# Optimization experiments

Hardware: AMD Instinct MI355X
Metric: run time of the kernel (lower is better)

The kernel has to match this reference:

```python
import jax, jax.numpy as jnp
import numpy as np

N = 30000      # nodes
IN = 768       # input feature dim
C = 128        # hidden channels (= conv out_dim, = gate dim)
HEADS = 4      # attention heads (TransformerConv and Semantic)
DH = 128       # per-head dim (concat=False -> out_channels)
R = 3          # num relations
E = 80000      # edges per relation
NEG = 0.01     # LeakyReLU slope


def setup_inputs() -> dict:
    key = jax.random.key(0)
    ks = iter(jax.random.split(key, 64))
    def nx(shape):
        return jax.random.normal(next(ks), shape, dtype=jnp.float32) * 0.02
    inp = {}
    inp["x"] = jax.random.normal(next(ks), (N, IN), dtype=jnp.float32)
    inp["edges"] = jax.random.randint(next(ks), (R, 2, E), 0, N, dtype=jnp.int32)
    inp["lin1_W"] = nx((IN, C)); inp["lin1_b"] = jnp.zeros((C,), jnp.float32)
    for l in ("l1", "l2"):
        inp[f"{l}_Wq"] = nx((R, C, HEADS * DH)); inp[f"{l}_bq"] = jnp.zeros((R, HEADS * DH), jnp.float32)
        inp[f"{l}_Wk"] = nx((R, C, HEADS * DH)); inp[f"{l}_bk"] = jnp.zeros((R, HEADS * DH), jnp.float32)
        inp[f"{l}_Wv"] = nx((R, C, HEADS * DH)); inp[f"{l}_bv"] = jnp.zeros((R, HEADS * DH), jnp.float32)
        inp[f"{l}_Ws"] = nx((R, C, DH));         inp[f"{l}_bs"] = jnp.zeros((R, DH), jnp.float32)
        inp[f"{l}_gW"] = nx((C + DH, C));        inp[f"{l}_gb"] = jnp.zeros((C,), jnp.float32)
        inp[f"{l}_sW1"] = nx((HEADS, C, C));     inp[f"{l}_sb1"] = jnp.zeros((HEADS, C), jnp.float32)
        inp[f"{l}_sw2"] = nx((HEADS, C))
    inp["lin2_W"] = nx((C, C)); inp["lin2_b"] = jnp.zeros((C,), jnp.float32)
    inp["clf_W"] = nx((C, 2)); inp["clf_b"] = jnp.zeros((2,), jnp.float32)
    return inp


def lrelu(x):
    return jnp.where(x >= 0, x, NEG * x)


def transformer_conv(x, src, dst, Wq, bq, Wk, bk, Wv, bv, Ws, bs):
    # PyG TransformerConv, heads=HEADS, concat=False (head mean), root_weight=True, eval (no dropout)
    n = x.shape[0]
    q = (x @ Wq + bq).reshape(n, HEADS, DH)
    k = (x @ Wk + bk).reshape(n, HEADS, DH)
    v = (x @ Wv + bv).reshape(n, HEADS, DH)
    logits = (q[dst] * k[src]).sum(-1) / np.sqrt(DH)      # [E, H]
    m = jax.ops.segment_max(logits, dst, num_segments=n)  # scatter-softmax (stable)
    a = jnp.exp(logits - m[dst])
    s = jax.ops.segment_sum(a, dst, num_segments=n)
    alpha = a / s[dst]
    agg = jax.ops.segment_sum(alpha[:, :, None] * v[src], dst, num_segments=n)  # [N, H, DH]
    return agg.mean(axis=1) + x @ Ws + bs


def semantic(Hm, sW1, sb1, sw2):
    # Hm: [N, R, C]; per-head scoring MLP -> softmax over relations -> weighted sum, averaged over heads
    t = jnp.tanh(jnp.einsum('nrc,hco->hnro', Hm, sW1) + sb1[:, None, None, :])  # [H, N, R, C]
    scores = jnp.einsum('hnro,ho->hnr', t, sw2).mean(axis=1)                    # [H, R]
    beta = jax.nn.softmax(scores, axis=-1)
    return jnp.einsum('hr,nrc->nc', beta, Hm) / HEADS


def rgt_layer(x, edges, Wq, bq, Wk, bk, Wv, bv, Ws, bs, gW, gb, sW1, sb1, sw2):
    Hs = []
    for r in range(R):  # small fixed relation loop
        src, dst = edges[r, 0], edges[r, 1]
        U = transformer_conv(x, src, dst, Wq[r], bq[r], Wk[r], bk[r], Wv[r], bv[r], Ws[r], bs[r])
        Z = jax.nn.sigmoid(jnp.concatenate([U, x], axis=1) @ gW + gb)
        Hs.append(jnp.tanh(U) * Z + x * (1.0 - Z))
    Hm = jnp.stack(Hs, axis=1)  # [N, R, C]
    return semantic(Hm, sW1, sb1, sw2)


def reference(x, edges, lin1_W, lin1_b,
              l1_Wq, l1_bq, l1_Wk, l1_bk, l1_Wv, l1_bv, l1_Ws, l1_bs, l1_gW, l1_gb, l1_sW1, l1_sb1, l1_sw2,
              l2_Wq, l2_bq, l2_Wk, l2_bk, l2_Wv, l2_bv, l2_Ws, l2_bs, l2_gW, l2_gb, l2_sW1, l2_sb1, l2_sw2,
              lin2_W, lin2_b, clf_W, clf_b):
    h = lrelu(x @ lin1_W + lin1_b)
    h = rgt_layer(h, edges, l1_Wq, l1_bq, l1_Wk, l1_bk, l1_Wv, l1_bv, l1_Ws, l1_bs, l1_gW, l1_gb, l1_sW1, l1_sb1, l1_sw2)
    h = rgt_layer(h, edges, l2_Wq, l2_bq, l2_Wk, l2_bk, l2_Wv, l2_bv, l2_Ws, l2_bs, l2_gW, l2_gb, l2_sW1, l2_sb1, l2_sw2)
    h = lrelu(h @ lin2_W + lin2_b)
    return h @ clf_W + clf_b
```

## Files before the change

kernel.cpp:

```cpp
#include <hip/hip_runtime.h>
#include <math.h>

#define Nn 30000
#define RR 3
#define EE 80000
#define MT_M 235

#define SAP 72
#define EP_LD 68
#define KBIG 0x40000000

typedef __attribute__((ext_vector_type(8))) short bf16x8;
typedef __attribute__((ext_vector_type(4))) float f32x4;

__device__ __forceinline__ unsigned short f2bf(float f) {
    union { float f; unsigned u; } v; v.f = f;
    unsigned r = v.u + 0x7fff + ((v.u >> 16) & 1);
    return (unsigned short)(r >> 16);
}
__device__ __forceinline__ float bf2f(short h) {
    union { unsigned u; float f; } v;
    v.u = ((unsigned)(unsigned short)h) << 16;
    return v.f;
}
__device__ __forceinline__ float fast_tanh(float x) {
    float e = __expf(2.f * x);
    return 1.f - 2.f / (e + 1.f);
}
__device__ __forceinline__ void unpack8(uint4 u, float* f) {
    union { unsigned u; float f; } a;
    a.u = u.x << 16;          f[0] = a.f;
    a.u = u.x & 0xffff0000u;  f[1] = a.f;
    a.u = u.y << 16;          f[2] = a.f;
    a.u = u.y & 0xffff0000u;  f[3] = a.f;
    a.u = u.z << 16;          f[4] = a.f;
    a.u = u.z & 0xffff0000u;  f[5] = a.f;
    a.u = u.w << 16;          f[6] = a.f;
    a.u = u.w & 0xffff0000u;  f[7] = a.f;
}

__device__ __forceinline__ void mfma_core(
    const short* __restrict__ A, int lda,
    const short* __restrict__ A2, int lda2, int ksplit,
    const short* __restrict__ Bt,
    int M, int K, int m0, int n0,
    short* As, short* Bs, f32x4 (&acc)[4][4])
{
    const int t = threadIdx.x;
    const int srow = t >> 3;
    const int scol = (t & 7) << 3;
    const int lane = t & 63;
    const int wave = t >> 6;
    const int wm = (wave >> 1) << 6;
    const int wn = (wave & 1) << 6;
    const int fr = lane & 15;
    const int quad = lane >> 4;

    for (int k0 = 0; k0 < K; k0 += 64) {
        const short* Abase; int kk0, ldax;
        if (k0 < ksplit) { Abase = A;  kk0 = k0;          ldax = lda;  }
        else             { Abase = A2; kk0 = k0 - ksplit; ldax = lda2; }
        #pragma unroll
        for (int rr = 0; rr < 4; rr++) {
            int r = srow + rr * 32;
            int gr = m0 + r;
            bf16x8 va = {0, 0, 0, 0, 0, 0, 0, 0};
            if (gr < M) va = *(const bf16x8*)(Abase + (size_t)gr * ldax + kk0 + scol);
            *(bf16x8*)(As + r * SAP + scol) = va;
        }
        #pragma unroll
        for (int rr = 0; rr < 4; rr++) {
            int r = srow + rr * 32;
            bf16x8 vb = *(const bf16x8*)(Bt + (size_t)(n0 + r) * K + k0 + scol);
            *(bf16x8*)(Bs + r * SAP + scol) = vb;
        }
        __syncthreads();
// ... 27 lines not shown
    __shared__ short As[128 * SAP];
    __shared__ short Bs[128 * SAP];
    f32x4 acc[4][4];
    #pragma unroll
    for (int i = 0; i < 4; i++)
        #pragma unroll
        for (int j = 0; j < 4; j++) acc[i][j] = (f32x4){0.f, 0.f, 0.f, 0.f};
    int m0 = blockIdx.y * 128, n0 = blockIdx.x * 128;
    mfma_core(A, lda, A2, lda2, ksplit, Bt, M, K, m0, n0, As, Bs, acc);

    const int t = threadIdx.x;
    const int lane = t & 63, wave = t >> 6;
    const int wm = (wave >> 1) << 6, wn = (wave & 1) << 6;
    const int fr = lane & 15, quad = lane >> 4;
    float* ws = (float*)As + wave * 16 * EP_LD;
    const int rrow = lane >> 2;
    const int cseg = (lane & 3) << 4;
    #pragma unroll
    for (int mi = 0; mi < 4; mi++) {
        #pragma unroll
        for (int ni = 0; ni < 4; ni++)
            #pragma unroll
            for (int reg = 0; reg < 4; reg++)
                ws[(quad * 4 + reg) * EP_LD + ni * 16 + fr] = acc[mi][ni][reg];
        int gr = m0 + wm + mi * 16 + rrow;
        if (gr >= M) continue;
        int gc = n0 + wn + cseg;
        float vals[16];
        #pragma unroll
        for (int j = 0; j < 16; j++) {
            float v = ws[rrow * EP_LD + cseg + j] + bias[gc + j];
            if (act == 1) v = (v >= 0.f) ? v : 0.01f * v;
            vals[j] = v;
        }
        if (C) {
            float* cp = C + (size_t)gr * ldc + gc;
            #pragma unroll
            for (int j4 = 0; j4 < 4; j4++)
                *(float4*)(cp + j4 * 4) = make_float4(vals[j4 * 4], vals[j4 * 4 + 1],
                                                      vals[j4 * 4 + 2], vals[j4 * 4 + 3]);
        }
        if (Cbf) {
            unsigned pk[8];
            #pragma unroll
            for (int j2 = 0; j2 < 8; j2++)
                pk[j2] = ((unsigned)f2bf(vals[2 * j2 + 1]) << 16) | (unsigned)f2bf(vals[2 * j2]);
            unsigned* bp = (unsigned*)(Cbf + (size_t)gr * ldcbf + gc);
            *(uint4*)bp       = make_uint4(pk[0], pk[1], pk[2], pk[3]);
            *(uint4*)(bp + 4) = make_uint4(pk[4], pk[5], pk[6], pk[7]);
        }
    }
}

__global__ __launch_bounds__(256) void gemm_qkvs(
    const short* __restrict__ A,
    const short* __restrict__ Wt, const float* __restrict__ bias,
    short* __restrict__ qkv3, short* __restrict__ Ubf, int M)
{
    __shared__ short As[128 * SAP];
    __shared__ short Bs[128 * SAP];
    f32x4 acc[4][4];
    #pragma unroll
    for (int i = 0; i < 4; i++)
        #pragma unroll
        for (int j = 0; j < 4; j++) acc[i][j] = (f32x4){0.f, 0.f, 0.f, 0.f};
    int m0 = blockIdx.y * 128, bx = blockIdx.x, n0 = bx * 128;
    mfma_core(A, 128, A, 128, KBIG, Wt, M, 128, m0, n0, As, Bs, acc);

    const int t = threadIdx.x;
    const int lane = t & 63, wave = t >> 6;
    const int wm = (wave >> 1) << 6, wn = (wave & 1) << 6;
    const int fr = lane & 15, quad = lane >> 4;
    float* ws = (float*)As + wave * 16 * EP_LD;
    const int rrow = lane >> 2;
    const int cseg = (lane & 3) << 4;
    #pragma unroll
    for (int mi = 0; mi < 4; mi++) {
        #pragma unroll
        for (int ni = 0; ni < 4; ni++)
            #pragma unroll
            for (int reg = 0; reg < 4; reg++)
                ws[(quad * 4 + reg) * EP_LD + ni * 16 + fr] = acc[mi][ni][reg];
        int gr = m0 + wm + mi * 16 + rrow;
        if (gr >= M) continue;
        int lc = wn + cseg;
        float vals[16];
        #pragma unroll
        for (int j = 0; j < 16; j++)
            vals[j] = ws[rrow * EP_LD + cseg + j] + bias[n0 + lc + j];
        unsigned pk[8];
        #pragma unroll
        for (int j2 = 0; j2 < 8; j2++)
            pk[j2] = ((unsigned)f2bf(vals[2 * j2 + 1]) << 16) | (unsigned)f2bf(vals[2 * j2]);
        short* dst;
        if (bx < 36) {
            int r = bx / 12;
            dst = qkv3 + ((size_t)(r * Nn + gr)) * 1536 + (bx - r * 12) * 128 + lc;
        } else {
            dst = Ubf + (size_t)gr * 384 + (bx - 36) * 128 + lc;
        }
        unsigned* bp = (unsigned*)dst;
        *(uint4*)bp       = make_uint4(pk[0], pk[1], pk[2], pk[3]);
        *(uint4*)(bp + 4) = make_uint4(pk[4], pk[5], pk[6], pk[7]);
    }
}

__global__ __launch_bounds__(256) void gate_mfma(
    const short* __restrict__ Ubf,
    const short* __restrict__ Hbf,
    const short* __restrict__ gWt, const float* __restrict__ gb,
    const float* __restrict__ Hf,
    float* __restrict__ Hm, short* __restrict__ HmBf,
    int M)
{
    __shared__ short As[128 * SAP];
    __shared__ short Bs[128 * SAP];
    f32x4 acc[4][4];
    #pragma unroll
    for (int i = 0; i < 4; i++)
        #pragma unroll
        for (int j = 0; j < 4; j++) acc[i][j] = (f32x4){0.f, 0.f, 0.f, 0.f};
    int r = blockIdx.z;
    int m0 = blockIdx.y * 128;
    mfma_core(Ubf + r * 128, 384, Hbf, 128, 128, gWt, M, 256, m0, 0, As, Bs, acc);

    const int t = threadIdx.x;
    const int lane = t & 63, wave = t >> 6;
    const int wm = (wave >> 1) << 6, wn = (wave & 1) << 6;
    const int fr = lane & 15, quad = lane >> 4;
    float* ws = (float*)As + wave * 16 * EP_LD;
    const int rrow = lane >> 2;
    const int cseg = (lane & 3) << 4;
    #pragma unroll
    for (int mi = 0; mi < 4; mi++) {
        #pragma unroll
        for (int ni = 0; ni < 4; ni++)
            #pragma unroll
            for (int reg = 0; reg < 4; reg++)
                ws[(quad * 4 + reg) * EP_LD + ni * 16 + fr] = acc[mi][ni][reg];
        int gr = m0 + wm + mi * 16 + rrow;
        if (gr >= M) continue;
        int gc = wn + cseg;
        const short* up = Ubf + (size_t)gr * 384 + r * 128 + gc;
        const float* hp = Hf + (size_t)gr * 128 + gc;
        float uv[16], hv[16];
        uint4 u0 = *(const uint4*)up;
        uint4 u1 = *(const uint4*)(up + 8);
        unpack8(u0, uv); unpack8(u1, uv + 8);
        #pragma unroll
        for (int j4 = 0; j4 < 4; j4++)
            *(float4*)(hv + j4 * 4) = *(const float4*)(hp + j4 * 4);
        float vals[16];
        #pragma unroll
        for (int j = 0; j < 16; j++) {
            float g = ws[rrow * EP_LD + cseg + j] + gb[gc + j];
            float z = 1.f / (1.f + __expf(-g));
// ... 80 lines not shown
            float e0 = __expf(s0 - mx), e1 = __expf(s1 - mx), e2 = __expf(s2 - mx);
            float inv = 1.f / (e0 + e1 + e2);
            wr[0] += 0.25f * e0 * inv;
            wr[1] += 0.25f * e1 * inv;
            wr[2] += 0.25f * e2 * inv;
        }
        w[0] = wr[0]; w[1] = wr[1]; w[2] = wr[2];
    }
}

__global__ void mix_kernel(const float* __restrict__ Hm, const float* __restrict__ w,
                           float* __restrict__ h, short* __restrict__ hbf, int total4)
{
    int i = blockIdx.x * blockDim.x + threadIdx.x;
    if (i >= total4) return;
    int n = i >> 5, c4 = (i & 31) << 2;
    const float* row = Hm + (size_t)n * 384 + c4;
    float4 a = *(const float4*)row;
    float4 b = *(const float4*)(row + 128);
    float4 c = *(const float4*)(row + 256);
    float w0 = w[0], w1 = w[1], w2 = w[2];
    float4 v = make_float4(w0 * a.x + w1 * b.x + w2 * c.x,
                           w0 * a.y + w1 * b.y + w2 * c.y,
                           w0 * a.z + w1 * b.z + w2 * c.z,
                           w0 * a.w + w1 * b.w + w2 * c.w);
    *(float4*)(h + (size_t)n * 128 + c4) = v;
    unsigned p0 = ((unsigned)f2bf(v.y) << 16) | (unsigned)f2bf(v.x);
    unsigned p1 = ((unsigned)f2bf(v.w) << 16) | (unsigned)f2bf(v.z);
    *(uint2*)(hbf + (size_t)n * 128 + c4) = make_uint2(p0, p1);
}

__global__ void convert_bf16_kernel(const float* __restrict__ src, unsigned* __restrict__ dst, int n_pairs)
{
    int i = blockIdx.x * blockDim.x + threadIdx.x;
    if (i >= n_pairs) return;
    float2 f = ((const float2*)src)[i];
    dst[i] = ((unsigned)f2bf(f.y) << 16) | (unsigned)f2bf(f.x);
}

__global__ void prep_global_kernel(const float* __restrict__ lin1_W, const float* __restrict__ lin2_W,
                                   short* __restrict__ lin1Wt, short* __restrict__ lin2Wt)
{
    int id = blockIdx.x * blockDim.x + threadIdx.x;
    if (id < 98304) {
        int n = id / 768, k = id % 768;
        lin1Wt[id] = (short)f2bf(lin1_W[k * 128 + n]);
    } else if (id < 114688) {
        int r = id - 98304;
        int n = r / 128, k = r % 128;
        lin2Wt[r] = (short)f2bf(lin2_W[k * 128 + n]);
    }
}

__global__ void prep_layer_kernel(
    const float* __restrict__ Wq, const float* __restrict__ Wk, const float* __restrict__ Wv,
    const float* __restrict__ Ws, const float* __restrict__ bq, const float* __restrict__ bk,
    const float* __restrict__ bv, const float* __restrict__ bs,
    const float* __restrict__ gW, const float* __restrict__ sW1,
    short* __restrict__ qkvsWt, short* __restrict__ gWt,
    short* __restrict__ sW1t, float* __restrict__ qkvsB)
{
    const int S0 = 638976;
    const int S1 = S0 + 32768;
    const int S2 = S1 + 65536;
    const int S3 = S2 + 4992;
    int id = blockIdx.x * blockDim.x + threadIdx.x;
    if (id < S0) {
        int n = id / 128, k = id - n * 128;
        float v;
        if (n < 4608) {
            int r = n / 1536, j = n - r * 1536;
            if (j < 512)       v = Wq[(size_t)r * 65536 + k * 512 + j];
            else if (j < 1024) v = Wk[(size_t)r * 65536 + k * 512 + (j - 512)];
            else               v = Wv[(size_t)r * 65536 + k * 512 + (j - 1024)];
        } else {
            int m = n - 4608;
            int r = m / 128, c = m - r * 128;
            v = Ws[(size_t)r * 16384 + k * 128 + c];
        }
        qkvsWt[id] = (short)f2bf(v);
    } else if (id < S1) {
        int q = id - S0;
        int n = q / 256, k = q - n * 256;
        gWt[q] = (short)f2bf(gW[k * 128 + n]);
    } else if (id < S2) {
        int q = id - S1;
        int h = q / 16384, rem = q - h * 16384;
        int n = rem / 128, k = rem - n * 128;
        sW1t[q] = (short)f2bf(sW1[(size_t)h * 16384 + k * 128 + n]);
    } else if (id < S3) {
        int q = id - S2;
        float v;
        if (q < 4608) {
            int r = q / 1536, j = q - r * 1536;
            if (j < 512)       v = bq[r * 512 + j];
            else if (j < 1024) v = bk[r * 512 + (j - 512)];
            else               v = bv[r * 512 + (j - 1024)];
        } else {
            v = bs[q - 4608];
        }
        qkvsB[q] = v;
    }
}

__global__ void zero_i32_kernel(int* __restrict__ p, int n)
{
    int i = blockIdx.x * blockDim.x + threadIdx.x;
    if (i < n) p[i] = 0;
}

__global__ void hist3_kernel(const int* __restrict__ edges, int* __restrict__ cnt3)
{
    int i = blockIdx.x * blockDim.x + threadIdx.x;
    if (i >= 3 * EE) return;
    int r = i / EE, e = i - r * EE;
    int d = edges[(size_t)r * 2 * EE + EE + e];
    atomicAdd(&cnt3[r * Nn + d], 1);
}

__global__ __launch_bounds__(1024) void scan3_kernel(const int* __restrict__ cnt3,
                                                     int* __restrict__ rowptr3)
{
    __shared__ int part[1024];
    const int r = blockIdx.x;
    const int* cnt = cnt3 + r * Nn;
    int* rowptr = rowptr3 + r * (Nn + 1);
    int tid = threadIdx.x;
    int per = (Nn + 1023) >> 10;
    int base = tid * per;
    int s = 0;
    for (int i = 0; i < per; i++) {
        int idx = base + i;
        if (idx < Nn) s += cnt[idx];
    }
    part[tid] = s;
    __syncthreads();
    for (int off = 1; off < 1024; off <<= 1) {
        int val = (tid >= off) ? part[tid - off] : 0;
        __syncthreads();
        part[tid] += val;
        __syncthreads();
    }
    int excl = (tid == 0) ? 0 : part[tid - 1];
    for (int i = 0; i < per; i++) {
        int idx = base + i;
        if (idx < Nn) { rowptr[idx] = excl; excl += cnt[idx]; }
    }
    if (tid == 1023) rowptr[Nn] = part[1023];
}

__global__ void scatter3_kernel(const int* __restrict__ edges,
                                const int* __restrict__ rowptr3, int* __restrict__ fill3,
                                int* __restrict__ col3)
{
    int i = blockIdx.x * blockDim.x + threadIdx.x;
    if (i >= 3 * EE) return;
    int r = i / EE, e = i - r * EE;
    int src = edges[(size_t)r * 2 * EE + e];
    int d   = edges[(size_t)r * 2 * EE + EE + e];
    int pos = rowptr3[r * (Nn + 1) + d] + atomicAdd(&fill3[r * Nn + d], 1);
    col3[r * EE + pos] = src;
}

__global__ __launch_bounds__(256) void attn_kernel(
    const short* __restrict__ qkv3,
    const int* __restrict__ rowptr3, const int* __restrict__ col3,
    short* __restrict__ Ubf)
{
    int wid = ((blockIdx.x * blockDim.x + threadIdx.x) >> 6);
    int lane = threadIdx.x & 63;
    if (wid >= 3 * Nn) return;
    int r = wid / Nn, n = wid - r * Nn;
    const short* qkv = qkv3 + (size_t)r * Nn * 1536;
    const int* rowptr = rowptr3 + r * (Nn + 1);
    const int* colb = col3 + r * EE;
    int beg = rowptr[n], end = rowptr[n + 1];

    uint4 qv = ((const uint4*)(qkv + (size_t)n * 1536))[lane];
    float qf[8];
    unpack8(qv, qf);

    float m = -INFINITY, s = 0.f;
    float acc[8] = {0.f, 0.f, 0.f, 0.f, 0.f, 0.f, 0.f, 0.f};
    const float scale = 0.088388347648318447f;

    for (int i = beg; i < end; i++) {
        int src = colb[i];
        const short* base = qkv + (size_t)src * 1536;
        uint4 kv4 = ((const uint4*)(base + 512))[lane];
        uint4 vv4 = ((const uint4*)(base + 1024))[lane];
        float kf[8];
        unpack8(kv4, kf);
        float p = qf[0] * kf[0] + qf[1] * kf[1] + qf[2] * kf[2] + qf[3] * kf[3]
                + qf[4] * kf[4] + qf[5] * kf[5] + qf[6] * kf[6] + qf[7] * kf[7];
        p += __shfl_xor(p, 1);
        p += __shfl_xor(p, 2);
        p += __shfl_xor(p, 4);
        p += __shfl_xor(p, 8);
        float l = p * scale;
        float nm = fmaxf(m, l);
        float sc = __expf(m - nm);
        float pe = __expf(l - nm);
        float vf[8];
        unpack8(vv4, vf);
        s = s * sc + pe;
        #pragma unroll
        for (int j = 0; j < 8; j++) acc[j] = acc[j] * sc + pe * vf[j];
        m = nm;
    }

    float inv = (s > 0.f) ? 1.f / s : 0.f;
    #pragma unroll
    for (int j = 0; j < 8; j++) acc[j] *= inv;
    #pragma unroll
    for (int j = 0; j < 8; j++) acc[j] += __shfl_xor(acc[j], 16);
    #pragma unroll
    for (int j = 0; j < 8; j++) acc[j] += __shfl_xor(acc[j], 32);

    if (lane < 16) {
        short* urow = Ubf + (size_t)n * 384 + r * 128 + lane * 8;
        uint4 old = *(uint4*)urow;
        float sv[8];
        unpack8(old, sv);
        #pragma unroll
        for (int j = 0; j < 8; j++) sv[j] += 0.25f * acc[j];
        unsigned p0 = ((unsigned)f2bf(sv[1]) << 16) | (unsigned)f2bf(sv[0]);
        unsigned p1 = ((unsigned)f2bf(sv[3]) << 16) | (unsigned)f2bf(sv[2]);
        unsigned p2 = ((unsigned)f2bf(sv[5]) << 16) | (unsigned)f2bf(sv[4]);
        unsigned p3 = ((unsigned)f2bf(sv[7]) << 16) | (unsigned)f2bf(sv[6]);
        *(uint4*)urow = make_uint4(p0, p1, p2, p3);
    }
}

__global__ void clf_kernel(const float* __restrict__ t, const float* __restrict__ W,
                           const float* __restrict__ b, float* __restrict__ out, int M)
{
    int n = blockIdx.x * blockDim.x + threadIdx.x;
    if (n >= M) return;
    const float* row = t + (size_t)n * 128;
    float a0 = b[0], a1 = b[1];
    #pragma unroll
    for (int kk = 0; kk < 128; kk++) {
        float a = row[kk];
        a0 += a * W[kk * 2];
        a1 += a * W[kk * 2 + 1];
    }
    out[n * 2] = a0;
    out[n * 2 + 1] = a1;
}

extern "C" void kernel_launch(void* const* d_in, const int* in_sizes, int n_in,
                              void* d_out, int out_size, void* d_ws, size_t ws_size,
                              hipStream_t stream)
{
    const float* x      = (const float*)d_in[0];
    const int*   edges  = (const int*)d_in[1];
    const float* lin1_W = (const float*)d_in[2];
    const float* lin1_b = (const float*)d_in[3];
    const int L0 = 4, L1 = 17;
    const float* lin2_W = (const float*)d_in[30];
    const float* lin2_b = (const float*)d_in[31];
    const float* clf_W  = (const float*)d_in[32];
    const float* clf_b  = (const float*)d_in[33];
    float* out = (float*)d_out;

    char* w = (char*)d_ws;
    size_t off = 0;
    auto alloc = [&](size_t bytes) { void* p = w + off; off = (off + bytes + 255) & ~(size_t)255; return p; };
    float* h      = (float*)alloc((size_t)Nn * 128 * 4);
    short* h_bf   = (short*)alloc((size_t)Nn * 128 * 2);
    short* U_bf   = (short*)alloc((size_t)Nn * 384 * 2);
    char* BIG     = (char*)alloc((size_t)3 * Nn * 1536 * 2);
    short* qkv3   = (short*)BIG;
    short* x_bf   = (short*)BIG;
    float* Hm     = (float*)BIG;
    short* Hm_bf  = (short*)(BIG + (size_t)Nn * 384 * 4);
    float* lin2o  = (float*)BIG;
    short* lin1Wt = (short*)alloc((size_t)98304 * 2);
    short* lin2Wt = (short*)alloc((size_t)16384 * 2);
    short* qkvsWt = (short*)alloc((size_t)2 * 638976 * 2);
    short* gWt    = (short*)alloc((size_t)2 * 32768 * 2);
    short* sW1t   = (short*)alloc((size_t)2 * 65536 * 2);
    float* qkvsB  = (float*)alloc((size_t)2 * 4992 * 4);
    int* rowptr3  = (int*)alloc((size_t)3 * (Nn + 1) * 4);
    int* cnt3     = (int*)alloc((size_t)3 * Nn * 4);
    int* col3     = (int*)alloc((size_t)3 * EE * 4);
    float* partial = (float*)alloc((size_t)12 * MT_M * 4);
    float* scores = (float*)alloc(12 * 4);
    float* wmix   = (float*)alloc(3 * 4);

    const int MT = MT_M;
    dim3 blk(256);

    {
        int n_pairs = Nn * 768 / 2;
        convert_bf16_kernel<<<(n_pairs + 255) / 256, blk, 0, stream>>>(x, (unsigned*)x_bf, n_pairs);
        prep_global_kernel<<<(114688 + 255) / 256, blk, 0, stream>>>(lin1_W, lin2_W, lin1Wt, lin2Wt);
        for (int l = 0; l < 2; l++) {
            int base = (l == 0) ? L0 : L1;
            prep_layer_kernel<<<(742272 + 255) / 256, blk, 0, stream>>>(
                (const float*)d_in[base + 0], (const float*)d_in[base + 2], (const float*)d_in[base + 4],
                (const float*)d_in[base + 6], (const float*)d_in[base + 1], (const float*)d_in[base + 3],
                (const float*)d_in[base + 5], (const float*)d_in[base + 7],
                (const float*)d_in[base + 8], (const float*)d_in[base + 10],
                qkvsWt + (size_t)l * 638976, gWt + (size_t)l * 32768,
                sW1t + (size_t)l * 65536, qkvsB + (size_t)l * 4992);
        }
        zero_i32_kernel<<<(3 * Nn + 255) / 256, blk, 0, stream>>>(cnt3, 3 * Nn);
        hist3_kernel<<<(3 * EE + 255) / 256, blk, 0, stream>>>(edges, cnt3);
        scan3_kernel<<<3, 1024, 0, stream>>>(cnt3, rowptr3);
        zero_i32_kernel<<<(3 * Nn + 255) / 256, blk, 0, stream>>>(cnt3, 3 * Nn);
        scatter3_kernel<<<(3 * EE + 255) / 256, blk, 0, stream>>>(edges, rowptr3, cnt3, col3);
    }

    gemm_mfma<<<dim3(1, MT), blk, 0, stream>>>(
        x_bf, 768, x_bf, 768, KBIG, lin1Wt, lin1_b, h, 128, h_bf, 128, Nn, 768, 1);

    for (int l = 0; l < 2; l++) {
        int base = (l == 0) ? L0 : L1;
        const float* gb  = (const float*)d_in[base + 9];
        const float* sb1 = (const float*)d_in[base + 11];
        const float* sw2 = (const float*)d_in[base + 12];
        short* lqkvsWt = qkvsWt + (size_t)l * 638976;
        short* lgWt    = gWt + (size_t)l * 32768;
        short* lsW1t   = sW1t + (size_t)l * 65536;
        float* lqkvsB  = qkvsB + (size_t)l * 4992;

        gemm_qkvs<<<dim3(39, MT), blk, 0, stream>>>(
            h_bf, lqkvsWt, lqkvsB, qkv3, U_bf, Nn);

        attn_kernel<<<(3 * Nn + 3) / 4, blk, 0, stream>>>(qkv3, rowptr3, col3, U_bf);

        gate_mfma<<<dim3(1, MT, 3), blk, 0, stream>>>(
            U_bf, h_bf, lgWt, gb, h, Hm, Hm_bf, Nn);

        semantic_mfma<<<dim3(4, MT, 3), blk, 0, stream>>>(Hm_bf, lsW1t, sb1, sw2, partial, Nn);
        reduce12_kernel<<<12, 64, 0, stream>>>(partial, scores);
        compute_w_kernel<<<1, 64, 0, stream>>>(scores, wmix, 1.f / (float)Nn);
        mix_kernel<<<(Nn * 32 + 255) / 256, blk, 0, stream>>>(Hm, wmix, h, h_bf, Nn * 32);
    }

    gemm_mfma<<<dim3(1, MT), blk, 0, stream>>>(
        h_bf, 128, h_bf, 128, KBIG, lin2Wt, lin2_b, lin2o, 128, (short*)nullptr, 0, Nn, 128, 1);
    clf_kernel<<<(Nn + 255) / 256, blk, 0, stream>>>(lin2o, clf_W, clf_b, out, Nn);
}
```

Baseline: 975.4 us.

## Keep QKVS weight tile in registers and loop over five row tiles per block

Replaces the LDS-staged QKVS projection GEMM with a register-resident version. Each block loads its 128x128 weight slice into registers once and reuses it across five 128-row tiles of the input. A fragments are read straight from global memory, which removes shared-memory staging and barriers. The epilogue writes bf16 directly from MFMA accumulators using swapped operands and the hardware packed convert. The cost is much higher register pressure (launch bounds of 256,2), fewer blocks, and direct global A loads that are less coalesced.

```diff
diff --git a/kernel.cpp b/kernel.cpp
--- a/kernel.cpp
+++ b/kernel.cpp
@@ -155,56 +155,95 @@
     }
 }
 
-__global__ __launch_bounds__(256) void gemm_qkvs(
+__global__ __launch_bounds__(256, 2) void gemm_qkvs_v2(
     const short* __restrict__ A,
-    const short* __restrict__ Wt, const float* __restrict__ bias,
+    const short* __restrict__ Bt,
+    const float* __restrict__ bias,
     short* __restrict__ qkv3, short* __restrict__ Ubf, int M)
 {
-    __shared__ short As[128 * SAP];
-    __shared__ short Bs[128 * SAP];
-    f32x4 acc[4][4];
-    #pragma unroll
-    for (int i = 0; i < 4; i++)
-        #pragma unroll
-        for (int j = 0; j < 4; j++) acc[i][j] = (f32x4){0.f, 0.f, 0.f, 0.f};
-    int m0 = blockIdx.y * 128, bx = blockIdx.x, n0 = bx * 128;
-    mfma_core(A, 128, A, 128, KBIG, Wt, M, 128, m0, n0, As, Bs, acc);
-
-    const int t = threadIdx.x;
-    const int lane = t & 63, wave = t >> 6;
-    const int wm = (wave >> 1) << 6, wn = (wave & 1) << 6;
-    const int fr = lane & 15, quad = lane >> 4;
-    float* ws = (float*)As + wave * 16 * EP_LD;
-    const int rrow = lane >> 2;
-    const int cseg = (lane & 3) << 4;
-    #pragma unroll
-    for (int mi = 0; mi < 4; mi++) {
-        #pragma unroll
-        for (int ni = 0; ni < 4; ni++)
-            #pragma unroll
-            for (int reg = 0; reg < 4; reg++)
-                ws[(quad * 4 + reg) * EP_LD + ni * 16 + fr] = acc[mi][ni][reg];
-        int gr = m0 + wm + mi * 16 + rrow;
-        if (gr >= M) continue;
-        int lc = wn + cseg;
-        float vals[16];
-        #pragma unroll
-        for (int j = 0; j < 16; j++)
-            vals[j] = ws[rrow * EP_LD + cseg + j] + bias[n0 + lc + j];
-        unsigned pk[8];
-        #pragma unroll
-        for (int j2 = 0; j2 < 8; j2++)
-            pk[j2] = ((unsigned)f2bf(vals[2 * j2 + 1]) << 16) | (unsigned)f2bf(vals[2 * j2]);
-        short* dst;
-        if (bx < 36) {
-            int r = bx / 12;
-            dst = qkv3 + ((size_t)(r * Nn + gr)) * 1536 + (bx - r * 12) * 128 + lc;
-        } else {
-            dst = Ubf + (size_t)gr * 384 + (bx - 36) * 128 + lc;
-        }
-        unsigned* bp = (unsigned*)dst;
-        *(uint4*)bp       = make_uint4(pk[0], pk[1], pk[2], pk[3]);
-        *(uint4*)(bp + 4) = make_uint4(pk[4], pk[5], pk[6], pk[7]);
+    const int tt = blockIdx.x;
+    const int n0 = tt * 128;
+    const int lane = threadIdx.x & 63;
+    const int wave = threadIdx.x >> 6;
+    const int wm = (wave >> 1) << 6;
+    const int wn = (wave & 1) << 6;
+    const int fr = lane & 15;
+    const int quad = lane >> 4;
+
+    bf16x8 bq[4][4];
+    #pragma unroll
+    for (int ni = 0; ni < 4; ni++)
+        #pragma unroll
+        for (int kc = 0; kc < 4; kc++)
+            bq[ni][kc] = *(const bf16x8*)(Bt + (size_t)(n0 + wn + ni * 16 + fr) * 128
+                                              + kc * 32 + quad * 8);
+
+    float4 b4[4];
+    #pragma unroll
+    for (int ni = 0; ni < 4; ni++)
+        b4[ni] = *(const float4*)(bias + n0 + wn + ni * 16 + quad * 4);
+
+    short* outBase;
+    size_t rowStride, colOff;
+    if (tt < 36) {
+        int r3 = tt / 12;
+        outBase = qkv3 + (size_t)r3 * Nn * 1536;
+        rowStride = 1536;
+        colOff = (size_t)(tt - r3 * 12) * 128;
+    } else {
+        outBase = Ubf;
+        rowStride = 384;
+        colOff = (size_t)(tt - 36) * 128;
+    }
+
+    #pragma unroll 1
+    for (int p = 0; p < 5; p++) {
+        const int m0 = (blockIdx.y * 5 + p) * 128;
+
+        bf16x8 af[4][4];
+        #pragma unroll
+        for (int mi = 0; mi < 4; mi++) {
+            int gr = m0 + wm + mi * 16 + fr;
+            #pragma unroll
+            for (int kc = 0; kc < 4; kc++) {
+                bf16x8 v = {0, 0, 0, 0, 0, 0, 0, 0};
+                if (gr < M) v = *(const bf16x8*)(A + (size_t)gr * 128 + kc * 32 + quad * 8);
+                af[mi][kc] = v;
+            }
+        }
+
+        f32x4 acc[4][4];
+        #pragma unroll
+        for (int i = 0; i < 4; i++)
+            #pragma unroll
+            for (int j = 0; j < 4; j++) acc[i][j] = (f32x4){0.f, 0.f, 0.f, 0.f};
+
+        #pragma unroll
+        for (int kc = 0; kc < 4; kc++)
+            #pragma unroll
+            for (int mi = 0; mi < 4; mi++)
+                #pragma unroll
+                for (int ni = 0; ni < 4; ni++)
+                    acc[mi][ni] = __builtin_amdgcn_mfma_f32_16x16x32_bf16(
+                        bq[ni][kc], af[mi][kc], acc[mi][ni], 0, 0, 0);
+
+        #pragma unroll
+        for (int mi = 0; mi < 4; mi++) {
+            int gr = m0 + wm + mi * 16 + fr;
+            if (gr >= M) continue;
+            short* dst = outBase + (size_t)gr * rowStride + colOff + wn;
+            #pragma unroll
+            for (int ni = 0; ni < 4; ni++) {
+                float v0 = acc[mi][ni][0] + b4[ni].x;
+                float v1 = acc[mi][ni][1] + b4[ni].y;
+                float v2 = acc[mi][ni][2] + b4[ni].z;
+                float v3 = acc[mi][ni][3] + b4[ni].w;
+                unsigned u0, u1;
+                asm("v_cvt_pk_bf16_f32 %0, %1, %2" : "=v"(u0) : "v"(v0), "v"(v1));
+                asm("v_cvt_pk_bf16_f32 %0, %1, %2" : "=v"(u1) : "v"(v2), "v"(v3));
+                *(uint2*)(dst + ni * 16 + quad * 4) = make_uint2(u0, u1);
+            }
+        }
     }
 }
 
@@ -665,7 +704,7 @@
         short* lsW1t   = sW1t + (size_t)l * 65536;
         float* lqkvsB  = qkvsB + (size_t)l * 4992;
 
-        gemm_qkvs<<<dim3(39, MT), blk, 0, stream>>>(
+        gemm_qkvs_v2<<<dim3(39, 47), blk, 0, stream>>>(
             h_bf, lqkvsWt, lqkvsB, qkv3, U_bf, Nn);
 
         attn_kernel<<<(3 * Nn + 3) / 4, blk, 0, stream>>>(qkv3, rowptr3, col3, U_bf);
```

Measured after the change: 1.013 ms. 3.9% more time.

## Reuse staged A tile across three output column tiles in QKV GEMM

Applied to the files above, without the earlier changes.

The QKV/skip projection GEMM now stages the 128x128 activation tile in shared memory once per block and loops over three 128-column weight tiles. It reads the B fragments straight from global memory into registers, so B no longer goes through shared memory. This cuts redundant A loads and launches a third as many blocks. In exchange there is less parallelism (13 blocks across instead of 39), higher register pressure from the held B fragments, and more shared memory per block.

```diff
diff --git a/kernel.cpp b/kernel.cpp
--- a/kernel.cpp
+++ b/kernel.cpp
@@ -8,6 +8,7 @@
 
 #define SAP 72
 #define EP_LD 68
+#define AS3 136
 #define KBIG 0x40000000
 
 typedef __attribute__((ext_vector_type(8))) short bf16x8;
@@ -155,56 +156,105 @@
     }
 }
 
-__global__ __launch_bounds__(256) void gemm_qkvs(
+__global__ __launch_bounds__(256) void gemm_qkvs_v3(
     const short* __restrict__ A,
-    const short* __restrict__ Wt, const float* __restrict__ bias,
+    const short* __restrict__ Bt,
+    const float* __restrict__ bias,
     short* __restrict__ qkv3, short* __restrict__ Ubf, int M)
 {
-    __shared__ short As[128 * SAP];
-    __shared__ short Bs[128 * SAP];
-    f32x4 acc[4][4];
-    #pragma unroll
-    for (int i = 0; i < 4; i++)
-        #pragma unroll
-        for (int j = 0; j < 4; j++) acc[i][j] = (f32x4){0.f, 0.f, 0.f, 0.f};
-    int m0 = blockIdx.y * 128, bx = blockIdx.x, n0 = bx * 128;
-    mfma_core(A, 128, A, 128, KBIG, Wt, M, 128, m0, n0, As, Bs, acc);
-
+    __shared__ short As[128 * AS3];
+    __shared__ float ws4[4 * 16 * EP_LD];
     const int t = threadIdx.x;
+    const int m0 = blockIdx.y * 128;
+
+    {
+        const int row0 = t >> 4;
+        const int col  = (t & 15) << 3;
+        #pragma unroll
+        for (int rr = 0; rr < 8; rr++) {
+            int r = row0 + rr * 16;
+            int gr = m0 + r;
+            bf16x8 va = {0, 0, 0, 0, 0, 0, 0, 0};
+            if (gr < M) va = *(const bf16x8*)(A + (size_t)gr * 128 + col);
+            *(bf16x8*)(As + r * AS3 + col) = va;
+        }
+    }
+    __syncthreads();
+
     const int lane = t & 63, wave = t >> 6;
     const int wm = (wave >> 1) << 6, wn = (wave & 1) << 6;
     const int fr = lane & 15, quad = lane >> 4;
-    float* ws = (float*)As + wave * 16 * EP_LD;
+    float* ws = ws4 + wave * 16 * EP_LD;
     const int rrow = lane >> 2;
     const int cseg = (lane & 3) << 4;
-    #pragma unroll
-    for (int mi = 0; mi < 4; mi++) {
+
+    #pragma unroll 1
+    for (int j = 0; j < 3; j++) {
+        const int tt = blockIdx.x * 3 + j;
+        const int n0 = tt * 128;
+
+        bf16x8 bq[4][4];
         #pragma unroll
         for (int ni = 0; ni < 4; ni++)
             #pragma unroll
-            for (int reg = 0; reg < 4; reg++)
-                ws[(quad * 4 + reg) * EP_LD + ni * 16 + fr] = acc[mi][ni][reg];
-        int gr = m0 + wm + mi * 16 + rrow;
-        if (gr >= M) continue;
-        int lc = wn + cseg;
-        float vals[16];
-        #pragma unroll
-        for (int j = 0; j < 16; j++)
-            vals[j] = ws[rrow * EP_LD + cseg + j] + bias[n0 + lc + j];
-        unsigned pk[8];
-        #pragma unroll
-        for (int j2 = 0; j2 < 8; j2++)
-            pk[j2] = ((unsigned)f2bf(vals[2 * j2 + 1]) << 16) | (unsigned)f2bf(vals[2 * j2]);
-        short* dst;
-        if (bx < 36) {
-            int r = bx / 12;
-            dst = qkv3 + ((size_t)(r * Nn + gr)) * 1536 + (bx - r * 12) * 128 + lc;
+            for (int kc = 0; kc < 4; kc++)
+                bq[ni][kc] = *(const bf16x8*)(Bt + (size_t)(n0 + wn + ni * 16 + fr) * 128
+                                                  + kc * 32 + quad * 8);
+
+        f32x4 acc[4][4];
+        #pragma unroll
+        for (int i = 0; i < 4; i++)
+            #pragma unroll
+            for (int jj = 0; jj < 4; jj++) acc[i][jj] = (f32x4){0.f, 0.f, 0.f, 0.f};
+
+        #pragma unroll
+        for (int kc = 0; kc < 4; kc++) {
+            bf16x8 af[4];
+            #pragma unroll
+            for (int mi = 0; mi < 4; mi++)
+                af[mi] = *(const bf16x8*)(As + (wm + mi * 16 + fr) * AS3 + kc * 32 + quad * 8);
+            #pragma unroll
+            for (int mi = 0; mi < 4; mi++)
+                #pragma unroll
+                for (int ni = 0; ni < 4; ni++)
+                    acc[mi][ni] = __builtin_amdgcn_mfma_f32_16x16x32_bf16(
+                        af[mi], bq[ni][kc], acc[mi][ni], 0, 0, 0);
+        }
+
+        short* outBase; size_t rowStride; int colOff;
+        if (tt < 36) {
+            int r3 = tt / 12;
+            outBase = qkv3 + (size_t)r3 * Nn * 1536;
+            rowStride = 1536;
+            colOff = (tt - r3 * 12) * 128;
         } else {
-            dst = Ubf + (size_t)gr * 384 + (bx - 36) * 128 + lc;
-        }
-        unsigned* bp = (unsigned*)dst;
-        *(uint4*)bp       = make_uint4(pk[0], pk[1], pk[2], pk[3]);
-        *(uint4*)(bp + 4) = make_uint4(pk[4], pk[5], pk[6], pk[7]);
+            outBase = Ubf;
+            rowStride = 384;
+            colOff = (tt - 36) * 128;
+        }
+
+        #pragma unroll
+        for (int mi = 0; mi < 4; mi++) {
+            #pragma unroll
+            for (int ni = 0; ni < 4; ni++)
+                #pragma unroll
+                for (int reg = 0; reg < 4; reg++)
+                    ws[(quad * 4 + reg) * EP_LD + ni * 16 + fr] = acc[mi][ni][reg];
+            int gr = m0 + wm + mi * 16 + rrow;
+            if (gr >= M) continue;
+            int lc = wn + cseg;
+            float vals[16];
+            #pragma unroll
+            for (int jj = 0; jj < 16; jj++)
+                vals[jj] = ws[rrow * EP_LD + cseg + jj] + bias[n0 + lc + jj];
+            unsigned pk[8];
+            #pragma unroll
+            for (int j2 = 0; j2 < 8; j2++)
+                pk[j2] = ((unsigned)f2bf(vals[2 * j2 + 1]) << 16) | (unsigned)f2bf(vals[2 * j2]);
+            unsigned* bp = (unsigned*)(outBase + (size_t)gr * rowStride + colOff + lc);
+            *(uint4*)bp       = make_uint4(pk[0], pk[1], pk[2], pk[3]);
+            *(uint4*)(bp + 4) = make_uint4(pk[4], pk[5], pk[6], pk[7]);
+        }
     }
 }
 
@@ -665,7 +715,7 @@
         short* lsW1t   = sW1t + (size_t)l * 65536;
         float* lqkvsB  = qkvsB + (size_t)l * 4992;
 
-        gemm_qkvs<<<dim3(39, MT), blk, 0, stream>>>(
+        gemm_qkvs_v3<<<dim3(13, MT), blk, 0, stream>>>(
             h_bf, lqkvsWt, lqkvsB, qkv3, U_bf, Nn);
 
         attn_kernel<<<(3 * Nn + 3) / 4, blk, 0, stream>>>(qkv3, rowptr3, col3, U_bf);
```

Result: slower. 1.008 ms (+3.4%).

## Fold Wq·Wkᵀ into a per-head query transform and defer the V projection until after aggregation

Applied to the files above, without the earlier changes.

The K and V projections are no longer computed per node. Per head, Wq and Wk are folded into one matrix (with the scale and bq term), so the GEMM emits q̂ = h·(Wq Wkᵀ) and attention dots q̂ directly against the raw 128-wide h rows of neighbours. The attention-weighted sum of h is stored per head. A new MFMA kernel then applies the head-averaged Wv, adding bv only for nodes that have in-edges. This cuts the QKV GEMM width and the per-edge gather bytes, at the cost of an extra GEMM pass over a 3×N×512 buffer and some bf16 rounding differences.

```diff
diff --git a/kernel.cpp b/kernel.cpp
--- a/kernel.cpp
+++ b/kernel.cpp
@@ -17,11 +17,6 @@
     union { float f; unsigned u; } v; v.f = f;
     unsigned r = v.u + 0x7fff + ((v.u >> 16) & 1);
     return (unsigned short)(r >> 16);
-}
-__device__ __forceinline__ float bf2f(short h) {
-    union { unsigned u; float f; } v;
-    v.u = ((unsigned)(unsigned short)h) << 16;
-    return v.f;
 }
 __device__ __forceinline__ float fast_tanh(float x) {
     float e = __expf(2.f * x);
@@ -155,10 +150,10 @@
     }
 }
 
-__global__ __launch_bounds__(256) void gemm_qkvs(
+__global__ __launch_bounds__(256) void gemm_qkvs_v4(
     const short* __restrict__ A,
     const short* __restrict__ Wt, const float* __restrict__ bias,
-    short* __restrict__ qkv3, short* __restrict__ Ubf, int M)
+    short* __restrict__ qhat3, short* __restrict__ Ubf, int M)
 {
     __shared__ short As[128 * SAP];
     __shared__ short Bs[128 * SAP];
@@ -196,13 +191,121 @@
         for (int j2 = 0; j2 < 8; j2++)
             pk[j2] = ((unsigned)f2bf(vals[2 * j2 + 1]) << 16) | (unsigned)f2bf(vals[2 * j2]);
         short* dst;
-        if (bx < 36) {
-            int r = bx / 12;
-            dst = qkv3 + ((size_t)(r * Nn + gr)) * 1536 + (bx - r * 12) * 128 + lc;
+        if (bx < 12) {
+            int r = bx >> 2;
+            dst = qhat3 + ((size_t)(r * Nn + gr)) * 512 + (bx - r * 4) * 128 + lc;
         } else {
-            dst = Ubf + (size_t)gr * 384 + (bx - 36) * 128 + lc;
+            dst = Ubf + (size_t)gr * 384 + (bx - 12) * 128 + lc;
         }
         unsigned* bp = (unsigned*)dst;
+        *(uint4*)bp       = make_uint4(pk[0], pk[1], pk[2], pk[3]);
+        *(uint4*)(bp + 4) = make_uint4(pk[4], pk[5], pk[6], pk[7]);
+    }
+}
+
+__global__ __launch_bounds__(256) void attn_v4(
+    const short* __restrict__ qhat3, const short* __restrict__ hbf,
+    const int* __restrict__ rowptr3, const int* __restrict__ col3,
+    short* __restrict__ Ah3)
+{
+    int wid = ((blockIdx.x * blockDim.x + threadIdx.x) >> 6);
+    int lane = threadIdx.x & 63;
+    if (wid >= 3 * Nn) return;
+    int r = wid / Nn, n = wid - r * Nn;
+    const int* rowptr = rowptr3 + r * (Nn + 1);
+    const int* colb = col3 + r * EE;
+    int beg = rowptr[n], end = rowptr[n + 1];
+
+    uint4 qv = ((const uint4*)(qhat3 + ((size_t)r * Nn + n) * 512))[lane];
+    float qf[8];
+    unpack8(qv, qf);
+    const int l16 = lane & 15;
+
+    float m = -INFINITY, s = 0.f;
+    float acc[8] = {0.f, 0.f, 0.f, 0.f, 0.f, 0.f, 0.f, 0.f};
+
+    for (int i = beg; i < end; i++) {
+        int src = colb[i];
+        uint4 hv = ((const uint4*)(hbf + (size_t)src * 128))[l16];
+        float hf[8];
+        unpack8(hv, hf);
+        float p = qf[0] * hf[0] + qf[1] * hf[1] + qf[2] * hf[2] + qf[3] * hf[3]
+                + qf[4] * hf[4] + qf[5] * hf[5] + qf[6] * hf[6] + qf[7] * hf[7];
+        p += __shfl_xor(p, 1);
+        p += __shfl_xor(p, 2);
+        p += __shfl_xor(p, 4);
+        p += __shfl_xor(p, 8);
+        float nm = fmaxf(m, p);
+        float sc = __expf(m - nm);
+        float pe = __expf(p - nm);
+        s = s * sc + pe;
+        #pragma unroll
+        for (int j = 0; j < 8; j++) acc[j] = acc[j] * sc + pe * hf[j];
+        m = nm;
+    }
+
+    float inv = (s > 0.f) ? 1.f / s : 0.f;
+    #pragma unroll
+    for (int j = 0; j < 8; j++) acc[j] *= inv;
+
+    unsigned p0 = ((unsigned)f2bf(acc[1]) << 16) | (unsigned)f2bf(acc[0]);
+    unsigned p1 = ((unsigned)f2bf(acc[3]) << 16) | (unsigned)f2bf(acc[2]);
+    unsigned p2 = ((unsigned)f2bf(acc[5]) << 16) | (unsigned)f2bf(acc[4]);
+    unsigned p3 = ((unsigned)f2bf(acc[7]) << 16) | (unsigned)f2bf(acc[6]);
+    *(uint4*)(Ah3 + ((size_t)r * Nn + n) * 512 + lane * 8) = make_uint4(p0, p1, p2, p3);
+}
+
+__global__ __launch_bounds__(256) void ufin_mfma(
+    const short* __restrict__ Ah3, const short* __restrict__ wvst,
+    const float* __restrict__ bvmean, const int* __restrict__ rowptr3,
+    short* __restrict__ U_bf, int M)
+{
+    __shared__ short As[128 * SAP];
+    __shared__ short Bs[128 * SAP];
+    f32x4 acc[4][4];
+    #pragma unroll
+    for (int i = 0; i < 4; i++)
+        #pragma unroll
+        for (int j = 0; j < 4; j++) acc[i][j] = (f32x4){0.f, 0.f, 0.f, 0.f};
+    int r = blockIdx.z;
+    int m0 = blockIdx.y * 128;
+    const short* Ar = Ah3 + (size_t)r * Nn * 512;
+    mfma_core(Ar, 512, Ar, 512, KBIG, wvst + r * 65536, M, 512, m0, 0, As, Bs, acc);
+
+    const int t = threadIdx.x;
+    const int lane = t & 63, wave = t >> 6;
+    const int wm = (wave >> 1) << 6, wn = (wave & 1) << 6;
+    const int fr = lane & 15, quad = lane >> 4;
+    float* ws = (float*)As + wave * 16 * EP_LD;
+    const int rrow = lane >> 2;
+    const int cseg = (lane & 3) << 4;
+    #pragma unroll
+    for (int mi = 0; mi < 4; mi++) {
+        #pragma unroll
+        for (int ni = 0; ni < 4; ni++)
+            #pragma unroll
+            for (int reg = 0; reg < 4; reg++)
+                ws[(quad * 4 + reg) * EP_LD + ni * 16 + fr] = acc[mi][ni][reg];
+        int gr = m0 + wm + mi * 16 + rrow;
+        if (gr >= M) continue;
+        int gc = wn + cseg;
+        int be = rowptr3[r * (Nn + 1) + gr];
+        int en = rowptr3[r * (Nn + 1) + gr + 1];
+        float mk = (en > be) ? 1.f : 0.f;
+        short* up = U_bf + (size_t)gr * 384 + r * 128 + gc;
+        uint4 u0 = *(const uint4*)up;
+        uint4 u1 = *(const uint4*)(up + 8);
+        float uv[16];
+        unpack8(u0, uv); unpack8(u1, uv + 8);
+        float vals[16];
+        #pragma unroll
+        for (int j = 0; j < 16; j++)
+            vals[j] = ws[rrow * EP_LD + cseg + j] + uv[j] + mk * bvmean[r * 128 + gc + j];
+        unsigned pk[8];
+        #pragma unroll
+        for (int j2 = 0; j2 < 8; j2++)
+            pk[j2] = ((unsigned)f2bf(vals[2 * j2 + 1]) << 16) | (unsigned)f2bf(vals[2 * j2]);
+        unsigned* bp = (unsigned*)up;
         *(uint4*)bp       = make_uint4(pk[0], pk[1], pk[2], pk[3]);
         *(uint4*)(bp + 4) = make_uint4(pk[4], pk[5], pk[6], pk[7]);
     }
@@ -391,33 +494,25 @@
     }
 }
 
-__global__ void prep_layer_kernel(
-    const float* __restrict__ Wq, const float* __restrict__ Wk, const float* __restrict__ Wv,
-    const float* __restrict__ Ws, const float* __restrict__ bq, const float* __restrict__ bk,
-    const float* __restrict__ bv, const float* __restrict__ bs,
+__global__ void prep_layer_v4(
+    const float* __restrict__ Ws, const float* __restrict__ bs,
     const float* __restrict__ gW, const float* __restrict__ sW1,
-    short* __restrict__ qkvsWt, short* __restrict__ gWt,
-    short* __restrict__ sW1t, float* __restrict__ qkvsB)
-{
-    const int S0 = 638976;
+    const float* __restrict__ Wv, const float* __restrict__ bv,
+    short* __restrict__ Wt4, short* __restrict__ gWt,
+    short* __restrict__ sW1t, short* __restrict__ wvst,
+    float* __restrict__ B4, float* __restrict__ bvmean)
+{
+    const int S0 = 49152;
     const int S1 = S0 + 32768;
     const int S2 = S1 + 65536;
-    const int S3 = S2 + 4992;
+    const int S3 = S2 + 196608;
+    const int S4 = S3 + 384;
+    const int S5 = S4 + 384;
     int id = blockIdx.x * blockDim.x + threadIdx.x;
     if (id < S0) {
         int n = id / 128, k = id - n * 128;
-        float v;
-        if (n < 4608) {
-            int r = n / 1536, j = n - r * 1536;
-            if (j < 512)       v = Wq[(size_t)r * 65536 + k * 512 + j];
-            else if (j < 1024) v = Wk[(size_t)r * 65536 + k * 512 + (j - 512)];
-            else               v = Wv[(size_t)r * 65536 + k * 512 + (j - 1024)];
-        } else {
-            int m = n - 4608;
-            int r = m / 128, c = m - r * 128;
-            v = Ws[(size_t)r * 16384 + k * 128 + c];
-        }
-        qkvsWt[id] = (short)f2bf(v);
+        int r = n >> 7, c = n & 127;
+        Wt4[(size_t)(1536 + n) * 128 + k] = (short)f2bf(Ws[(size_t)r * 16384 + k * 128 + c]);
     } else if (id < S1) {
         int q = id - S0;
         int n = q / 256, k = q - n * 256;
@@ -429,16 +524,55 @@
         sW1t[q] = (short)f2bf(sW1[(size_t)h * 16384 + k * 128 + n]);
     } else if (id < S3) {
         int q = id - S2;
-        float v;
-        if (q < 4608) {
-            int r = q / 1536, j = q - r * 1536;
-            if (j < 512)       v = bq[r * 512 + j];
-            else if (j < 1024) v = bk[r * 512 + (j - 512)];
-            else               v = bv[r * 512 + (j - 1024)];
-        } else {
-            v = bs[q - 4608];
-        }
-        qkvsB[q] = v;
+        int r = q / 65536, rem = q - r * 65536;
+        int d = rem / 512, mcol = rem - d * 512;
+        int hh = mcol >> 7, j = mcol & 127;
+        wvst[q] = (short)f2bf(0.25f * Wv[(size_t)r * 65536 + j * 512 + hh * 128 + d]);
+    } else if (id < S4) {
+        int q = id - S3;
+        B4[1536 + q] = bs[q];
+    } else if (id < S5) {
+        int q = id - S4;
+        int r = q >> 7, d = q & 127;
+        bvmean[q] = 0.25f * (bv[r * 512 + d] + bv[r * 512 + 128 + d]
+                           + bv[r * 512 + 256 + d] + bv[r * 512 + 384 + d]);
+    }
+}
+
+__global__ __launch_bounds__(256) void gmat_kernel(
+    const float* __restrict__ Wq0, const float* __restrict__ Wk0, const float* __restrict__ bq0,
+    const float* __restrict__ Wq1, const float* __restrict__ Wk1, const float* __restrict__ bq1,
+    short* __restrict__ Wt4, float* __restrict__ B4)
+{
+    __shared__ float WqL[128 * 128];
+    __shared__ float WkL[128 * 128];
+    int h = blockIdx.x, r = blockIdx.y, l = blockIdx.z;
+    const float* Wq = l ? Wq1 : Wq0;
+    const float* Wk = l ? Wk1 : Wk0;
+    const float* bq = l ? bq1 : bq0;
+    short* Wt = Wt4 + (size_t)l * 245760;
+    float* Bb = B4 + l * 1920;
+    const float scale = 0.088388347648318447f;
+    int t = threadIdx.x;
+    for (int idx = t; idx < 16384; idx += 256) {
+        int a = idx >> 7, b = idx & 127;
+        WqL[idx] = Wq[(size_t)r * 65536 + b * 512 + h * 128 + a];
+        WkL[idx] = Wk[(size_t)r * 65536 + a * 512 + h * 128 + b];
+    }
+    __syncthreads();
+    for (int out = t; out < 16384; out += 256) {
+        int i = out & 127, j = out >> 7;
+        float dot = 0.f;
+        #pragma unroll 8
+        for (int d = 0; d < 128; d++)
+            dot += WqL[d * 128 + i] * WkL[j * 128 + d];
+        Wt[(size_t)(r * 512 + h * 128 + j) * 128 + i] = (short)f2bf(scale * dot);
+    }
+    if (t < 128) {
+        const float* bqh = bq + r * 512 + h * 128;
+        float c = 0.f;
+        for (int d = 0; d < 128; d++) c += bqh[d] * WkL[t * 128 + d];
+        Bb[r * 512 + h * 128 + t] = scale * c;
     }
 }
 
@@ -501,76 +635,6 @@
     col3[r * EE + pos] = src;
 }
 
-__global__ __launch_bounds__(256) void attn_kernel(
-    const short* __restrict__ qkv3,
-    const int* __restrict__ rowptr3, const int* __restrict__ col3,
-    short* __restrict__ Ubf)
-{
-    int wid = ((blockIdx.x * blockDim.x + threadIdx.x) >> 6);
-    int lane = threadIdx.x & 63;
-    if (wid >= 3 * Nn) return;
-    int r = wid / Nn, n = wid - r * Nn;
-    const short* qkv = qkv3 + (size_t)r * Nn * 1536;
-    const int* rowptr = rowptr3 + r * (Nn + 1);
-    const int* colb = col3 + r * EE;
-    int beg = rowptr[n], end = rowptr[n + 1];
-
-    uint4 qv = ((const uint4*)(qkv + (size_t)n * 1536))[lane];
-    float qf[8];
-    unpack8(qv, qf);
-
-    float m = -INFINITY, s = 0.f;
-    float acc[8] = {0.f, 0.f, 0.f, 0.f, 0.f, 0.f, 0.f, 0.f};
-    const float scale = 0.088388347648318447f;
-
-    for (int i = beg; i < end; i++) {
-        int src = colb[i];
-        const short* base = qkv + (size_t)src * 1536;
-        uint4 kv4 = ((const uint4*)(base + 512))[lane];
-        uint4 vv4 = ((const uint4*)(base + 1024))[lane];
-        float kf[8];
-        unpack8(kv4, kf);
-        float p = qf[0] * kf[0] + qf[1] * kf[1] + qf[2] * kf[2] + qf[3] * kf[3]
-                + qf[4] * kf[4] + qf[5] * kf[5] + qf[6] * kf[6] + qf[7] * kf[7];
-        p += __shfl_xor(p, 1);
-        p += __shfl_xor(p, 2);
-        p += __shfl_xor(p, 4);
-        p += __shfl_xor(p, 8);
-        float l = p * scale;
-        float nm = fmaxf(m, l);
-        float sc = __expf(m - nm);
-        float pe = __expf(l - nm);
-        float vf[8];
-        unpack8(vv4, vf);
-        s = s * sc + pe;
-        #pragma unroll
-        for (int j = 0; j < 8; j++) acc[j] = acc[j] * sc + pe * vf[j];
-        m = nm;
-    }
-
-    float inv = (s > 0.f) ? 1.f / s : 0.f;
-    #pragma unroll
-    for (int j = 0; j < 8; j++) acc[j] *= inv;
-    #pragma unroll
-    for (int j = 0; j < 8; j++) acc[j] += __shfl_xor(acc[j], 16);
-    #pragma unroll
-    for (int j = 0; j < 8; j++) acc[j] += __shfl_xor(acc[j], 32);
-
-    if (lane < 16) {
-        short* urow = Ubf + (size_t)n * 384 + r * 128 + lane * 8;
-        uint4 old = *(uint4*)urow;
-        float sv[8];
-        unpack8(old, sv);
-        #pragma unroll
-        for (int j = 0; j < 8; j++) sv[j] += 0.25f * acc[j];
-        unsigned p0 = ((unsigned)f2bf(sv[1]) << 16) | (unsigned)f2bf(sv[0]);
-        unsigned p1 = ((unsigned)f2bf(sv[3]) << 16) | (unsigned)f2bf(sv[2]);
-        unsigned p2 = ((unsigned)f2bf(sv[5]) << 16) | (unsigned)f2bf(sv[4]);
-        unsigned p3 = ((unsigned)f2bf(sv[7]) << 16) | (unsigned)f2bf(sv[6]);
-        *(uint4*)urow = make_uint4(p0, p1, p2, p3);
-    }
-}
-
 __global__ void clf_kernel(const float* __restrict__ t, const float* __restrict__ W,
                            const float* __restrict__ b, float* __restrict__ out, int M)
 {
@@ -609,18 +673,22 @@
     float* h      = (float*)alloc((size_t)Nn * 128 * 4);
     short* h_bf   = (short*)alloc((size_t)Nn * 128 * 2);
     short* U_bf   = (short*)alloc((size_t)Nn * 384 * 2);
-    char* BIG     = (char*)alloc((size_t)3 * Nn * 1536 * 2);
-    short* qkv3   = (short*)BIG;
+    const size_t QH = (size_t)3 * Nn * 512 * 2;
+    char* BIG     = (char*)alloc(2 * QH);
+    short* qhat3  = (short*)BIG;
+    short* Ah3    = (short*)(BIG + QH);
     short* x_bf   = (short*)BIG;
     float* Hm     = (float*)BIG;
     short* Hm_bf  = (short*)(BIG + (size_t)Nn * 384 * 4);
     float* lin2o  = (float*)BIG;
     short* lin1Wt = (short*)alloc((size_t)98304 * 2);
     short* lin2Wt = (short*)alloc((size_t)16384 * 2);
-    short* qkvsWt = (short*)alloc((size_t)2 * 638976 * 2);
+    short* qkvsWt4 = (short*)alloc((size_t)2 * 245760 * 2);
     short* gWt    = (short*)alloc((size_t)2 * 32768 * 2);
     short* sW1t   = (short*)alloc((size_t)2 * 65536 * 2);
-    float* qkvsB  = (float*)alloc((size_t)2 * 4992 * 4);
+    short* wvst   = (short*)alloc((size_t)2 * 196608 * 2);
+    float* qkvsB4 = (float*)alloc((size_t)2 * 1920 * 4);
+    float* bvmean = (float*)alloc((size_t)2 * 384 * 4);
     int* rowptr3  = (int*)alloc((size_t)3 * (Nn + 1) * 4);
     int* cnt3     = (int*)alloc((size_t)3 * Nn * 4);
     int* col3     = (int*)alloc((size_t)3 * EE * 4);
@@ -637,14 +705,18 @@
         prep_global_kernel<<<(114688 + 255) / 256, blk, 0, stream>>>(lin1_W, lin2_W, lin1Wt, lin2Wt);
         for (int l = 0; l < 2; l++) {
             int base = (l == 0) ? L0 : L1;
-            prep_layer_kernel<<<(742272 + 255) / 256, blk, 0, stream>>>(
-                (const float*)d_in[base + 0], (const float*)d_in[base + 2], (const float*)d_in[base + 4],
-                (const float*)d_in[base + 6], (const float*)d_in[base + 1], (const float*)d_in[base + 3],
-                (const float*)d_in[base + 5], (const float*)d_in[base + 7],
+            prep_layer_v4<<<(344832 + 255) / 256, blk, 0, stream>>>(
+                (const float*)d_in[base + 6], (const float*)d_in[base + 7],
                 (const float*)d_in[base + 8], (const float*)d_in[base + 10],
-                qkvsWt + (size_t)l * 638976, gWt + (size_t)l * 32768,
-                sW1t + (size_t)l * 65536, qkvsB + (size_t)l * 4992);
-        }
+                (const float*)d_in[base + 4], (const float*)d_in[base + 5],
+                qkvsWt4 + (size_t)l * 245760, gWt + (size_t)l * 32768,
+                sW1t + (size_t)l * 65536, wvst + (size_t)l * 196608,
+                qkvsB4 + (size_t)l * 1920, bvmean + (size_t)l * 384);
+        }
+        gmat_kernel<<<dim3(4, 3, 2), blk, 0, stream>>>(
+            (const float*)d_in[L0 + 0], (const float*)d_in[L0 + 2], (const float*)d_in[L0 + 1],
+            (const float*)d_in[L1 + 0], (const float*)d_in[L1 + 2], (const float*)d_in[L1 + 1],
+            qkvsWt4, qkvsB4);
         zero_i32_kernel<<<(3 * Nn + 255) / 256, blk, 0, stream>>>(cnt3, 3 * Nn);
         hist3_kernel<<<(3 * EE + 255) / 256, blk, 0, stream>>>(edges, cnt3);
         scan3_kernel<<<3, 1024, 0, stream>>>(cnt3, rowptr3);
@@ -660,15 +732,19 @@
         const float* gb  = (const float*)d_in[base + 9];
         const float* sb1 = (const float*)d_in[base + 11];
         const float* sw2 = (const float*)d_in[base + 12];
-        short* lqkvsWt = qkvsWt + (size_t)l * 638976;
-        short* lgWt    = gWt + (size_t)l * 32768;
-        short* lsW1t   = sW1t + (size_t)l * 65536;
-        float* lqkvsB  = qkvsB + (size_t)l * 4992;
-
-        gemm_qkvs<<<dim3(39, MT), blk, 0, stream>>>(
-            h_bf, lqkvsWt, lqkvsB, qkv3, U_bf, Nn);
-
-        attn_kernel<<<(3 * Nn + 3) / 4, blk, 0, stream>>>(qkv3, rowptr3, col3, U_bf);
+        short* lWt4   = qkvsWt4 + (size_t)l * 245760;
+        short* lgWt   = gWt + (size_t)l * 32768;
+        short* lsW1t  = sW1t + (size_t)l * 65536;
+        short* lwvst  = wvst + (size_t)l * 196608;
+        float* lB4    = qkvsB4 + (size_t)l * 1920;
+        float* lbvm   = bvmean + (size_t)l * 384;
+
+        gemm_qkvs_v4<<<dim3(15, MT), blk, 0, stream>>>(
+            h_bf, lWt4, lB4, qhat3, U_bf, Nn);
+
+        attn_v4<<<(3 * Nn + 3) / 4, blk, 0, stream>>>(qhat3, h_bf, rowptr3, col3, Ah3);
+
+        ufin_mfma<<<dim3(1, MT, 3), blk, 0, stream>>>(Ah3, lwvst, lbvm, rowptr3, U_bf, Nn);
 
         gate_mfma<<<dim3(1, MT, 3), blk, 0, stream>>>(
             U_bf, h_bf, lgWt, gb, h, Hm, Hm_bf, Nn);
```

Result: faster. 907.5 us (-7.0%).
